# Kernel tuning notes

Hardware: AMD Instinct MI355X
Metric: run time of the kernel (lower is better)

## Reference

```python
import jax, jax.numpy as jnp
import numpy as np

TAU = 0.1
SELF_MASK = 1e6  # added to diagonal of self-distances (y_neg is x)


def _cdist(a, b):
    # pairwise L2 distances, [Na, Nb]; eps keeps sqrt grad finite at 0
    sq = (a * a).sum(-1)[:, None] + (b * b).sum(-1)[None, :] - 2.0 * (a @ b.T)
    return jnp.sqrt(jnp.maximum(sq, 1e-12))


def setup_inputs() -> dict:
    key = jax.random.key(0)
    k1, k2 = jax.random.split(key)
    N, D = 4096, 512
    return {
        "x": jax.random.normal(k1, (N, D), dtype=jnp.float32),
        "y_pos": jax.random.normal(k2, (N, D), dtype=jnp.float32),
    }


def reference(x, y_pos):
    # compute_drift_velocity with y_neg = x (training/loss path)
    N = x.shape[0]
    dist_pos = _cdist(x, y_pos)                      # [N, N]
    dist_neg = _cdist(x, x) + SELF_MASK * jnp.eye(N, dtype=x.dtype)
    logits = -jnp.concatenate([dist_pos, dist_neg], axis=1) / TAU  # [N, 2N]
    # dual normalization: row softmax * column softmax, geometric mean
    A_row = jax.nn.softmax(logits, axis=-1)
    A_col = jax.nn.softmax(logits, axis=0)
    A = jnp.sqrt(A_row * A_col)
    A_pos, A_neg = A[:, :N], A[:, N:]
    drift = A_pos @ y_pos - A_neg @ x                # [N, D]
    return drift
```

## Files before the change

kernel.cpp:

```cpp
#include <hip/hip_runtime.h>
#include <math.h>

#define NN   4096
#define DD   512
#define TWON 8192
#define KSLICE 8

typedef _Float16 half_t;
typedef unsigned short u16;
using half8  = __attribute__((ext_vector_type(8))) half_t;
using short8 = __attribute__((ext_vector_type(8))) short;
using f32x4  = __attribute__((ext_vector_type(4))) float;

__device__ __forceinline__ u16 f2bf(float f) {
    unsigned u = __float_as_uint(f);
    u += 0x7fffu + ((u >> 16) & 1u);
    return (u16)(u >> 16);
}
__device__ __forceinline__ float bf2f(u16 h) {
    return __uint_as_float(((unsigned)h) << 16);
}
__device__ __forceinline__ void gl16(const void* g, void* l) {
    __builtin_amdgcn_global_load_lds(
        (const __attribute__((address_space(1))) void*)g,
        (__attribute__((address_space(3))) void*)l, 16, 0, 0);
}
__device__ __forceinline__ f32x4 mfma16h(half8 a, half8 b, f32x4 c) {
    return __builtin_amdgcn_mfma_f32_16x16x32_f16(a, b, c, 0, 0, 0);
}
__device__ __forceinline__ f32x4 mfma16b(short8 a, short8 b, f32x4 c) {
    return __builtin_amdgcn_mfma_f32_16x16x32_bf16(a, b, c, 0, 0, 0);
}

__global__ __launch_bounds__(64)
void prep_k(const float* __restrict__ x, const float* __restrict__ y,
            half_t* __restrict__ bhi, float* __restrict__ nb) {
    int r = blockIdx.x;
    int l = threadIdx.x;
    const float* src = (r < NN) ? (y + (size_t)r * DD) : (x + (size_t)(r - NN) * DD);
    float4 v0 = *reinterpret_cast<const float4*>(src + l * 8);
    float4 v1 = *reinterpret_cast<const float4*>(src + l * 8 + 4);
    float e[8] = {v0.x, v0.y, v0.z, v0.w, v1.x, v1.y, v1.z, v1.w};
    float s = 0.f;
    half8 h;
    #pragma unroll
    for (int q = 0; q < 8; ++q) {
        s += e[q] * e[q];
        h[q] = (half_t)e[q];
    }
    *reinterpret_cast<half8*>(bhi + (size_t)r * DD + l * 8) = h;
    #pragma unroll
    for (int off = 32; off; off >>= 1) s += __shfl_down(s, off);
    if (l == 0) nb[r] = s;
}

__global__ __launch_bounds__(256)
void b2t_k(const float* __restrict__ x, const float* __restrict__ y, u16* __restrict__ b2t) {
    __shared__ float tl[32][33];
    int k0 = blockIdx.x * 32, d0 = blockIdx.y * 32;
    int tx = threadIdx.x, ty = threadIdx.y;
    const float* src = (k0 < NN) ? y : x;
    int row0 = (k0 < NN) ? k0 : (k0 - NN);
    #pragma unroll
    for (int j = 0; j < 4; ++j)
        tl[ty + 8 * j][tx] = src[(size_t)(row0 + ty + 8 * j) * DD + d0 + tx];
    __syncthreads();
    float sgn = (k0 < NN) ? 1.f : -1.f;
    #pragma unroll
    for (int j = 0; j < 4; ++j) {
        float v = tl[tx][ty + 8 * j] * sgn;
        b2t[(size_t)(d0 + ty + 8 * j) * TWON + k0 + tx] = f2bf(v);
    }
}

__global__ __launch_bounds__(256)
void gemm1_k(const half_t* __restrict__ bhi,
             const float* __restrict__ nb, u16* __restrict__ Ef,
             float* __restrict__ Ct,
             float* __restrict__ rpm, float* __restrict__ rps,
             float* __restrict__ cpm, float* __restrict__ cps) {
    __shared__ unsigned char lds[32768];
    const int t = threadIdx.x;
    const int wave = t >> 6, lane = t & 63;
    const int i0 = blockIdx.y * 128, j0 = blockIdx.x * 128;
    const int wm = (wave >> 1) * 64, wn = (wave & 1) * 64;
    const half_t* ahig = bhi + (size_t)NN * DD;
    f32x4 acc[4][4] = {};
    for (int k0 = 0; k0 < DD; k0 += 64) {
        __syncthreads();
        #pragma unroll
        for (int q = 0; q < 4; ++q) {
            const int dbase = (wave * 4 + q) * 1024;
            const int p  = dbase + lane * 16;
            const int r  = p >> 7;
            const int cb = (p & 127) ^ ((r & 7) << 4);
            const size_t offA = (size_t)(i0 + r) * DD + k0 + (cb >> 1);
            const size_t offB = (size_t)(j0 + r) * DD + k0 + (cb >> 1);
            gl16(ahig + offA, lds + dbase);
            gl16(bhi  + offB, lds + 16384 + dbase);
        }
        asm volatile("s_waitcnt vmcnt(0)" ::: "memory");
        __builtin_amdgcn_sched_barrier(0);
        __syncthreads();
        #pragma unroll
        for (int kk = 0; kk < 2; ++kk) {
            half8 ah[4];
            #pragma unroll
            for (int m = 0; m < 4; ++m) {
                const int row = wm + m * 16 + (lane & 15);
                const int off = row * 128 + ((kk * 64 + (lane >> 4) * 16) ^ ((row & 7) << 4));
                ah[m] = *reinterpret_cast<const half8*>(lds + off);
            }
            #pragma unroll
            for (int n = 0; n < 4; ++n) {
                const int row = wn + n * 16 + (lane & 15);
                const int off = row * 128 + ((kk * 64 + (lane >> 4) * 16) ^ ((row & 7) << 4));
                half8 bh = *reinterpret_cast<const half8*>(lds + 16384 + off);
                #pragma unroll
                for (int m = 0; m < 4; ++m)
                    acc[m][n] = mfma16h(ah[m], bh, acc[m][n]);
            }
        }
    }
    float nbj[4];
    #pragma unroll
    for (int n = 0; n < 4; ++n) nbj[n] = nb[j0 + wn + n * 16 + (lane & 15)];
    float tmax = -3.0e38f;
    #pragma unroll
    for (int m = 0; m < 4; ++m) {
        #pragma unroll
        for (int r4 = 0; r4 < 4; ++r4) {
            const int i = i0 + wm + m * 16 + (lane >> 4) * 4 + r4;
            const float nxi = nb[NN + i];
            #pragma unroll
            for (int n = 0; n < 4; ++n) {
                const int j = j0 + wn + n * 16 + (lane & 15);
                float sq = nxi + nbj[n] - 2.0f * acc[m][n][r4];
                float lg = -10.0f * sqrtf(fmaxf(sq, 1e-12f));
                if (j == i + NN) lg = -1e7f;
                acc[m][n][r4] = lg;
                tmax = fmaxf(tmax, lg);
            }
        }
    }
    #pragma unroll
    for (int off = 1; off < 64; off <<= 1) tmax = fmaxf(tmax, __shfl_xor(tmax, off));
    __syncthreads();
    float* red = reinterpret_cast<float*>(lds);
    if (lane == 0) red[wave] = tmax;
    __syncthreads();
    const float C = fmaxf(fmaxf(red[0], red[1]), fmaxf(red[2], red[3]));
    __syncthreads();
    if (t == 0) Ct[blockIdx.y * 64 + blockIdx.x] = C;
    float rs[16] = {}, cs[4] = {};
    #pragma unroll
    for (int m = 0; m < 4; ++m)
        #pragma unroll
        for (int r4 = 0; r4 < 4; ++r4) {
            const int idx = m * 4 + r4;
            const int i = i0 + wm + m * 16 + (lane >> 4) * 4 + r4;
            #pragma unroll
            for (int n = 0; n < 4; ++n) {
                const int j = j0 + wn + n * 16 + (lane & 15);
                float e = __expf(acc[m][n][r4] - C);
                Ef[(size_t)i * TWON + j] = f2bf(e);
                rs[idx] += e;
                cs[n]   += e;
            }
        }
    #pragma unroll
    for (int off = 1; off < 16; off <<= 1) {
        #pragma unroll
        for (int idx = 0; idx < 16; ++idx) rs[idx] += __shfl_xor(rs[idx], off);
    }
    #pragma unroll
    for (int off = 16; off < 64; off <<= 1) {
        #pragma unroll
        for (int n = 0; n < 4; ++n) cs[n] += __shfl_xor(cs[n], off);
    }
    if ((lane & 15) == 0) {
        #pragma unroll
        for (int m = 0; m < 4; ++m)
            #pragma unroll
            for (int r4 = 0; r4 < 4; ++r4) {
                const int r = wm + m * 16 + (lane >> 4) * 4 + r4;
                red[(wave & 1) * 128 + r] = rs[m * 4 + r4];
            }
    }
    if (lane < 16) {
        #pragma unroll
        for (int n = 0; n < 4; ++n) {
            const int c = wn + n * 16 + lane;
            red[256 + (wave >> 1) * 128 + c] = cs[n];
        }
    }
    __syncthreads();
    if (t < 128) {
        float S = red[t] + red[128 + t];
        rpm[(size_t)blockIdx.x * NN + i0 + t] = C;
        rps[(size_t)blockIdx.x * NN + i0 + t] = S;
    } else {
        const int c = t - 128;
        float S = red[256 + c] + red[384 + c];
        cpm[(size_t)blockIdx.y * TWON + j0 + c] = C;
        cps[(size_t)blockIdx.y * TWON + j0 + c] = S;
    }
}

__global__ __launch_bounds__(256)
void row_comb_k(const float* __restrict__ rpm, const float* __restrict__ rps,
                float* __restrict__ rm, float* __restrict__ rrs) {
    int i = blockIdx.x * 256 + threadIdx.x;
    float M = -3.0e38f;
    for (int tt = 0; tt < TWON / 128; ++tt) M = fmaxf(M, rpm[(size_t)tt * NN + i]);
    float S = 0.f;
    for (int tt = 0; tt < TWON / 128; ++tt)
        S += rps[(size_t)tt * NN + i] * __expf(rpm[(size_t)tt * NN + i] - M);
    rm[i] = M; rrs[i] = rsqrtf(S);
}

__global__ __launch_bounds__(256)
void col_comb_k(const float* __restrict__ cpm, const float* __restrict__ cps,
                float* __restrict__ Pj) {
    int j = blockIdx.x * 256 + threadIdx.x;
    float M = -3.0e38f;
    for (int tt = 0; tt < NN / 128; ++tt) M = fmaxf(M, cpm[(size_t)tt * TWON + j]);
    float S = 0.f;
    for (int tt = 0; tt < NN / 128; ++tt)
        S += cps[(size_t)tt * TWON + j] * __expf(cpm[(size_t)tt * TWON + j] - M);
    Pj[j] = -0.5f * M - 0.5f * logf(S);
}

__global__ __launch_bounds__(512, 4)
void gemm2_k(const u16* __restrict__ Ef, const u16* __restrict__ b2t,
             const float* __restrict__ Ct, const float* __restrict__ rm,
             const float* __restrict__ Pj, const float* __restrict__ rrs,
             float* __restrict__ part) {
    __shared__ unsigned char lds[16384];
    const int t = threadIdx.x;
    const int wave = t >> 6, lane = t & 63;
    const int sw = blockIdx.x;
    const int kslice = sw & 7;
    const int i0 = (sw >> 3) * 64;
    const int ib = (sw >> 3) >> 1;
    const int kbase = kslice * (TWON / KSLICE);
    const int wn = wave * 64;
    const int sr = t >> 3;
    const int kc = (t & 7) * 8;
    const int awbyte = sr * 128 + ((kc * 2) ^ ((sr & 7) << 4));
    const int NT = (TWON / KSLICE) / 64;
    const float rmh = 0.5f * rm[i0 + sr];
    f32x4 acc[4][4] = {};
    short8 aE;
    float4 p0, p1;
    float arg;
    auto LOADA = [&](int it) {
        const int k = kbase + it * 64 + kc;
        aE = *reinterpret_cast<const short8*>(Ef + (size_t)(i0 + sr) * TWON + k);
        p0 = *reinterpret_cast<const float4*>(Pj + k);
        p1 = *reinterpret_cast<const float4*>(Pj + k + 4);
        arg = Ct[ib * 64 + ((kbase + it * 64) >> 7)] - rmh;
    };
    auto STOREA = [&](int buf) {
        short8 g;
        g[0] = (short)f2bf(bf2f((u16)aE[0]) * __expf(arg + p0.x));
        g[1] = (short)f2bf(bf2f((u16)aE[1]) * __expf(arg + p0.y));
        g[2] = (short)f2bf(bf2f((u16)aE[2]) * __expf(arg + p0.z));
        g[3] = (short)f2bf(bf2f((u16)aE[3]) * __expf(arg + p0.w));
        g[4] = (short)f2bf(bf2f((u16)aE[4]) * __expf(arg + p1.x));
        g[5] = (short)f2bf(bf2f((u16)aE[5]) * __expf(arg + p1.y));
        g[6] = (short)f2bf(bf2f((u16)aE[6]) * __expf(arg + p1.z));
        g[7] = (short)f2bf(bf2f((u16)aE[7]) * __expf(arg + p1.w));
        *reinterpret_cast<short8*>(lds + buf * 8192 + awbyte) = g;
    };
    LOADA(0);
    STOREA(0);
    __syncthreads();
    int cur = 0;
    for (int it = 0; it < NT; ++it) {
        short8 bfr0[4], bfr1[4];
        #pragma unroll
        for (int n = 0; n < 4; ++n) {
            const int d = wn + n * 16 + (lane & 15);
            const u16* bp = b2t + (size_t)d * TWON + kbase + it * 64 + (lane >> 4) * 8;
            bfr0[n] = *reinterpret_cast<const short8*>(bp);
            bfr1[n] = *reinterpret_cast<const short8*>(bp + 32);
        }
        if (it + 1 < NT) LOADA(it + 1);
        #pragma unroll
        for (int kk = 0; kk < 2; ++kk) {
            short8 af[4];
            #pragma unroll
            for (int m = 0; m < 4; ++m) {
                const int row = m * 16 + (lane & 15);
                const int off = cur * 8192 + row * 128 +
                                ((kk * 64 + (lane >> 4) * 16) ^ ((row & 7) << 4));
                af[m] = *reinterpret_cast<const short8*>(lds + off);
            }
            #pragma unroll
            for (int m = 0; m < 4; ++m)
                #pragma unroll
                for (int n = 0; n < 4; ++n)
                    acc[m][n] = mfma16b(af[m], (kk == 0) ? bfr0[n] : bfr1[n], acc[m][n]);
        }
        if (it + 1 < NT) STOREA(cur ^ 1);
        __syncthreads();
        cur ^= 1;
    }
    float* pout = part + (size_t)kslice * NN * DD;
    #pragma unroll
    for (int m = 0; m < 4; ++m) {
        float rf[4];
        #pragma unroll
        for (int r4 = 0; r4 < 4; ++r4) rf[r4] = rrs[i0 + m * 16 + (lane >> 4) * 4 + r4];
        #pragma unroll
        for (int n = 0; n < 4; ++n) {
            const int d = wn + n * 16 + (lane & 15);
            #pragma unroll
            for (int r4 = 0; r4 < 4; ++r4) {
                const int i = i0 + m * 16 + (lane >> 4) * 4 + r4;
                pout[(size_t)i * DD + d] = acc[m][n][r4] * rf[r4];
            }
        }
    }
}

__global__ __launch_bounds__(256)
void reduce_k(const float* __restrict__ part, float* __restrict__ out) {
    const size_t e4 = ((size_t)blockIdx.x * 256 + threadIdx.x) * 4;
    float4 a = *reinterpret_cast<const float4*>(part + e4);
    #pragma unroll
    for (int s = 1; s < KSLICE; ++s) {
        float4 b = *reinterpret_cast<const float4*>(part + (size_t)s * NN * DD + e4);
        a.x += b.x; a.y += b.y; a.z += b.z; a.w += b.w;
    }
    *reinterpret_cast<float4*>(out + e4) = a;
}

extern "C" void kernel_launch(void* const* d_in, const int* in_sizes, int n_in,
                              void* d_out, int out_size, void* d_ws, size_t ws_size,
                              hipStream_t stream) {
    const float* x = (const float*)d_in[0];
    const float* y = (const float*)d_in[1];
    float* out = (float*)d_out;

    char* w = (char*)d_ws;
    const size_t OFF_EF   = 0;
    const size_t OFF_BHI  = 67108864;
    const size_t OFF_B2T  = OFF_BHI + 8388608;
    const size_t OFF_PART = OFF_B2T + 8388608;
    const size_t OFF_RPM  = OFF_PART + 67108864;
    const size_t OFF_RPS  = OFF_RPM + 1048576;
    const size_t OFF_CPM  = OFF_RPS + 1048576;
    const size_t OFF_CPS  = OFF_CPM + 1048576;
    const size_t OFF_CT   = OFF_CPS + 1048576;
    const size_t OFF_TAIL = OFF_CT + 65536;

    u16*    Ef   = (u16*)(w + OFF_EF);
    half_t* bhi  = (half_t*)(w + OFF_BHI);
    u16*    b2t  = (u16*)(w + OFF_B2T);
    float*  part = (float*)(w + OFF_PART);
    float*  rpm  = (float*)(w + OFF_RPM);
    float*  rps  = (float*)(w + OFF_RPS);
    float*  cpm  = (float*)(w + OFF_CPM);
    float*  cps  = (float*)(w + OFF_CPS);
    float*  Ct   = (float*)(w + OFF_CT);
    float*  nb   = (float*)(w + OFF_TAIL);
    float*  rm   = nb  + TWON;
    float*  rrs  = rm  + NN;
    float*  Pj   = rrs + NN;

    prep_k<<<TWON, 64, 0, stream>>>(x, y, bhi, nb);
    gemm1_k<<<dim3(TWON / 128, NN / 128), 256, 0, stream>>>(bhi, nb, Ef, Ct,
                                                            rpm, rps, cpm, cps);
    row_comb_k<<<NN / 256, 256, 0, stream>>>(rpm, rps, rm, rrs);
    col_comb_k<<<TWON / 256, 256, 0, stream>>>(cpm, cps, Pj);
    b2t_k<<<dim3(TWON / 32, DD / 32), dim3(32, 8), 0, stream>>>(x, y, b2t);
    gemm2_k<<<512, 512, 0, stream>>>(Ef, b2t, Ct, rm, Pj, rrs, part);
    reduce_k<<<(NN * DD / 4) / 256, 256, 0, stream>>>(part, out);
}
```

Baseline: 188.8 us.

## Store split-K partials in fp16 and unroll gemm2 loop by two

The split-K partial sums written by gemm2 are now stored as fp16 instead of fp32, halving the write and read traffic between gemm2 and the reduction kernel. The reduction kernel now handles 8 elements per thread. The gemm2 main loop is also unrolled by two with separate A-register sets, so the prefetch for a later step overlaps the current MFMA work without a buffer index variable. Storing partials in fp16 reduces accuracy and may overflow if partial values are large.

```diff
diff --git a/kernel.cpp b/kernel.cpp
--- a/kernel.cpp
+++ b/kernel.cpp
@@ -235,7 +235,7 @@
 void gemm2_k(const u16* __restrict__ Ef, const u16* __restrict__ b2t,
              const float* __restrict__ Ct, const float* __restrict__ rm,
              const float* __restrict__ Pj, const float* __restrict__ rrs,
-             float* __restrict__ part) {
+             half_t* __restrict__ part) {
     __shared__ unsigned char lds[16384];
     const int t = threadIdx.x;
     const int wave = t >> 6, lane = t & 63;
@@ -251,49 +251,64 @@
     const int NT = (TWON / KSLICE) / 64;
     const float rmh = 0.5f * rm[i0 + sr];
     f32x4 acc[4][4] = {};
-    short8 aE;
-    float4 p0, p1;
-    float arg;
-    auto LOADA = [&](int it) {
+    short8 aE_A, aE_B;
+    float4 pA0, pA1, pB0, pB1;
+    float argA, argB;
+    auto LOADA_A = [&](int it) {
         const int k = kbase + it * 64 + kc;
-        aE = *reinterpret_cast<const short8*>(Ef + (size_t)(i0 + sr) * TWON + k);
-        p0 = *reinterpret_cast<const float4*>(Pj + k);
-        p1 = *reinterpret_cast<const float4*>(Pj + k + 4);
-        arg = Ct[ib * 64 + ((kbase + it * 64) >> 7)] - rmh;
-    };
-    auto STOREA = [&](int buf) {
+        aE_A = *reinterpret_cast<const short8*>(Ef + (size_t)(i0 + sr) * TWON + k);
+        pA0 = *reinterpret_cast<const float4*>(Pj + k);
+        pA1 = *reinterpret_cast<const float4*>(Pj + k + 4);
+        argA = Ct[ib * 64 + ((kbase + it * 64) >> 7)] - rmh;
+    };
+    auto LOADA_B = [&](int it) {
+        const int k = kbase + it * 64 + kc;
+        aE_B = *reinterpret_cast<const short8*>(Ef + (size_t)(i0 + sr) * TWON + k);
+        pB0 = *reinterpret_cast<const float4*>(Pj + k);
+        pB1 = *reinterpret_cast<const float4*>(Pj + k + 4);
+        argB = Ct[ib * 64 + ((kbase + it * 64) >> 7)] - rmh;
+    };
+    auto STOREA_A = [&](int buf) {
         short8 g;
-        g[0] = (short)f2bf(bf2f((u16)aE[0]) * __expf(arg + p0.x));
-        g[1] = (short)f2bf(bf2f((u16)aE[1]) * __expf(arg + p0.y));
-        g[2] = (short)f2bf(bf2f((u16)aE[2]) * __expf(arg + p0.z));
-        g[3] = (short)f2bf(bf2f((u16)aE[3]) * __expf(arg + p0.w));
-        g[4] = (short)f2bf(bf2f((u16)aE[4]) * __expf(arg + p1.x));
-        g[5] = (short)f2bf(bf2f((u16)aE[5]) * __expf(arg + p1.y));
-        g[6] = (short)f2bf(bf2f((u16)aE[6]) * __expf(arg + p1.z));
-        g[7] = (short)f2bf(bf2f((u16)aE[7]) * __expf(arg + p1.w));
+        g[0] = (short)f2bf(bf2f((u16)aE_A[0]) * __expf(argA + pA0.x));
+        g[1] = (short)f2bf(bf2f((u16)aE_A[1]) * __expf(argA + pA0.y));
+        g[2] = (short)f2bf(bf2f((u16)aE_A[2]) * __expf(argA + pA0.z));
+        g[3] = (short)f2bf(bf2f((u16)aE_A[3]) * __expf(argA + pA0.w));
+        g[4] = (short)f2bf(bf2f((u16)aE_A[4]) * __expf(argA + pA1.x));
+        g[5] = (short)f2bf(bf2f((u16)aE_A[5]) * __expf(argA + pA1.y));
+        g[6] = (short)f2bf(bf2f((u16)aE_A[6]) * __expf(argA + pA1.z));
+        g[7] = (short)f2bf(bf2f((u16)aE_A[7]) * __expf(argA + pA1.w));
         *reinterpret_cast<short8*>(lds + buf * 8192 + awbyte) = g;
     };
-    LOADA(0);
-    STOREA(0);
-    __syncthreads();
-    int cur = 0;
-    for (int it = 0; it < NT; ++it) {
-        short8 bfr0[4], bfr1[4];
+    auto STOREA_B = [&](int buf) {
+        short8 g;
+        g[0] = (short)f2bf(bf2f((u16)aE_B[0]) * __expf(argB + pB0.x));
+        g[1] = (short)f2bf(bf2f((u16)aE_B[1]) * __expf(argB + pB0.y));
+        g[2] = (short)f2bf(bf2f((u16)aE_B[2]) * __expf(argB + pB0.z));
+        g[3] = (short)f2bf(bf2f((u16)aE_B[3]) * __expf(argB + pB0.w));
+        g[4] = (short)f2bf(bf2f((u16)aE_B[4]) * __expf(argB + pB1.x));
+        g[5] = (short)f2bf(bf2f((u16)aE_B[5]) * __expf(argB + pB1.y));
+        g[6] = (short)f2bf(bf2f((u16)aE_B[6]) * __expf(argB + pB1.z));
+        g[7] = (short)f2bf(bf2f((u16)aE_B[7]) * __expf(argB + pB1.w));
+        *reinterpret_cast<short8*>(lds + buf * 8192 + awbyte) = g;
+    };
+    auto BLOAD = [&](int it, short8* b0, short8* b1) {
         #pragma unroll
         for (int n = 0; n < 4; ++n) {
             const int d = wn + n * 16 + (lane & 15);
             const u16* bp = b2t + (size_t)d * TWON + kbase + it * 64 + (lane >> 4) * 8;
-            bfr0[n] = *reinterpret_cast<const short8*>(bp);
-            bfr1[n] = *reinterpret_cast<const short8*>(bp + 32);
-        }
-        if (it + 1 < NT) LOADA(it + 1);
+            b0[n] = *reinterpret_cast<const short8*>(bp);
+            b1[n] = *reinterpret_cast<const short8*>(bp + 32);
+        }
+    };
+    auto DOMFMA = [&](int buf, short8* b0, short8* b1) {
         #pragma unroll
         for (int kk = 0; kk < 2; ++kk) {
             short8 af[4];
             #pragma unroll
             for (int m = 0; m < 4; ++m) {
                 const int row = m * 16 + (lane & 15);
-                const int off = cur * 8192 + row * 128 +
+                const int off = buf * 8192 + row * 128 +
                                 ((kk * 64 + (lane >> 4) * 16) ^ ((row & 7) << 4));
                 af[m] = *reinterpret_cast<const short8*>(lds + off);
             }
@@ -301,13 +316,27 @@
             for (int m = 0; m < 4; ++m)
                 #pragma unroll
                 for (int n = 0; n < 4; ++n)
-                    acc[m][n] = mfma16b(af[m], (kk == 0) ? bfr0[n] : bfr1[n], acc[m][n]);
-        }
-        if (it + 1 < NT) STOREA(cur ^ 1);
+                    acc[m][n] = mfma16b(af[m], (kk == 0) ? b0[n] : b1[n], acc[m][n]);
+        }
+    };
+    LOADA_A(0);
+    LOADA_B(1);
+    STOREA_A(0);
+    __syncthreads();
+    for (int it = 0; it < NT; it += 2) {
+        short8 bfr0[4], bfr1[4];
+        BLOAD(it, bfr0, bfr1);
+        if (it + 2 < NT) LOADA_A(it + 2);
+        DOMFMA(0, bfr0, bfr1);
+        STOREA_B(1);
         __syncthreads();
-        cur ^= 1;
-    }
-    float* pout = part + (size_t)kslice * NN * DD;
+        BLOAD(it + 1, bfr0, bfr1);
+        if (it + 3 < NT) LOADA_B(it + 3);
+        DOMFMA(1, bfr0, bfr1);
+        if (it + 2 < NT) STOREA_A(0);
+        __syncthreads();
+    }
+    half_t* pout = part + (size_t)kslice * NN * DD;
     #pragma unroll
     for (int m = 0; m < 4; ++m) {
         float rf[4];
@@ -319,22 +348,24 @@
             #pragma unroll
             for (int r4 = 0; r4 < 4; ++r4) {
                 const int i = i0 + m * 16 + (lane >> 4) * 4 + r4;
-                pout[(size_t)i * DD + d] = acc[m][n][r4] * rf[r4];
+                pout[(size_t)i * DD + d] = (half_t)(acc[m][n][r4] * rf[r4]);
             }
         }
     }
 }
 
 __global__ __launch_bounds__(256)
-void reduce_k(const float* __restrict__ part, float* __restrict__ out) {
-    const size_t e4 = ((size_t)blockIdx.x * 256 + threadIdx.x) * 4;
-    float4 a = *reinterpret_cast<const float4*>(part + e4);
-    #pragma unroll
-    for (int s = 1; s < KSLICE; ++s) {
-        float4 b = *reinterpret_cast<const float4*>(part + (size_t)s * NN * DD + e4);
-        a.x += b.x; a.y += b.y; a.z += b.z; a.w += b.w;
-    }
-    *reinterpret_cast<float4*>(out + e4) = a;
+void reduce_k(const half_t* __restrict__ part, float* __restrict__ out) {
+    const size_t e8 = ((size_t)blockIdx.x * 256 + threadIdx.x) * 8;
+    float s[8] = {};
+    #pragma unroll
+    for (int sl = 0; sl < KSLICE; ++sl) {
+        half8 v = *reinterpret_cast<const half8*>(part + (size_t)sl * NN * DD + e8);
+        #pragma unroll
+        for (int q = 0; q < 8; ++q) s[q] += (float)v[q];
+    }
+    *reinterpret_cast<float4*>(out + e8)     = make_float4(s[0], s[1], s[2], s[3]);
+    *reinterpret_cast<float4*>(out + e8 + 4) = make_float4(s[4], s[5], s[6], s[7]);
 }
 
 extern "C" void kernel_launch(void* const* d_in, const int* in_sizes, int n_in,
@@ -359,7 +390,7 @@
     u16*    Ef   = (u16*)(w + OFF_EF);
     half_t* bhi  = (half_t*)(w + OFF_BHI);
     u16*    b2t  = (u16*)(w + OFF_B2T);
-    float*  part = (float*)(w + OFF_PART);
+    half_t* part = (half_t*)(w + OFF_PART);
     float*  rpm  = (float*)(w + OFF_RPM);
     float*  rps  = (float*)(w + OFF_RPS);
     float*  cpm  = (float*)(w + OFF_CPM);
@@ -377,5 +408,5 @@
     col_comb_k<<<TWON / 256, 256, 0, stream>>>(cpm, cps, Pj);
     b2t_k<<<dim3(TWON / 32, DD / 32), dim3(32, 8), 0, stream>>>(x, y, b2t);
     gemm2_k<<<512, 512, 0, stream>>>(Ef, b2t, Ct, rm, Pj, rrs, part);
-    reduce_k<<<(NN * DD / 4) / 256, 256, 0, stream>>>(part, out);
-}
+    reduce_k<<<(NN * DD / 8) / 256, 256, 0, stream>>>(part, out);
+}
```

Result: slower. 210.5 us (+11.5%).

## Store split-K partials as packed bf16 in fragment order and read fp16 copy for transpose

Applied to the files above, without the earlier changes.

The split-K partial sums from gemm2 are now written as packed bf16 in a per-thread fragment-contiguous layout with 16-byte stores, which halves partial traffic and replaces strided scalar fp32 stores. The reduce kernel is rewritten to read that layout and scatter fp32 results to the output. The transpose kernel now reads the existing fp16 copy instead of fp32 inputs, halving its read volume. Partials in bf16 lose precision before the final sum, and the transpose now converts fp16 to bf16 rather than fp32 to bf16.

```diff
diff --git a/kernel.cpp b/kernel.cpp
--- a/kernel.cpp
+++ b/kernel.cpp
@@ -55,20 +55,18 @@
 }
 
 __global__ __launch_bounds__(256)
-void b2t_k(const float* __restrict__ x, const float* __restrict__ y, u16* __restrict__ b2t) {
-    __shared__ float tl[32][33];
+void b2tr_k(const half_t* __restrict__ bhi, u16* __restrict__ b2t) {
+    __shared__ half_t tl[32][33];
     int k0 = blockIdx.x * 32, d0 = blockIdx.y * 32;
     int tx = threadIdx.x, ty = threadIdx.y;
-    const float* src = (k0 < NN) ? y : x;
-    int row0 = (k0 < NN) ? k0 : (k0 - NN);
     #pragma unroll
     for (int j = 0; j < 4; ++j)
-        tl[ty + 8 * j][tx] = src[(size_t)(row0 + ty + 8 * j) * DD + d0 + tx];
+        tl[ty + 8 * j][tx] = bhi[(size_t)(k0 + ty + 8 * j) * DD + d0 + tx];
     __syncthreads();
     float sgn = (k0 < NN) ? 1.f : -1.f;
     #pragma unroll
     for (int j = 0; j < 4; ++j) {
-        float v = tl[tx][ty + 8 * j] * sgn;
+        float v = (float)tl[tx][ty + 8 * j] * sgn;
         b2t[(size_t)(d0 + ty + 8 * j) * TWON + k0 + tx] = f2bf(v);
     }
 }
@@ -235,7 +233,7 @@
 void gemm2_k(const u16* __restrict__ Ef, const u16* __restrict__ b2t,
              const float* __restrict__ Ct, const float* __restrict__ rm,
              const float* __restrict__ Pj, const float* __restrict__ rrs,
-             float* __restrict__ part) {
+             unsigned* __restrict__ part) {
     __shared__ unsigned char lds[16384];
     const int t = threadIdx.x;
     const int wave = t >> 6, lane = t & 63;
@@ -307,34 +305,54 @@
         __syncthreads();
         cur ^= 1;
     }
-    float* pout = part + (size_t)kslice * NN * DD;
+    unsigned* pout = part + ((size_t)(kslice * 64 + (sw >> 3)) * 512 + t) * 32;
     #pragma unroll
     for (int m = 0; m < 4; ++m) {
         float rf[4];
         #pragma unroll
         for (int r4 = 0; r4 < 4; ++r4) rf[r4] = rrs[i0 + m * 16 + (lane >> 4) * 4 + r4];
+        unsigned pk[8];
         #pragma unroll
         for (int n = 0; n < 4; ++n) {
-            const int d = wn + n * 16 + (lane & 15);
-            #pragma unroll
-            for (int r4 = 0; r4 < 4; ++r4) {
-                const int i = i0 + m * 16 + (lane >> 4) * 4 + r4;
-                pout[(size_t)i * DD + d] = acc[m][n][r4] * rf[r4];
-            }
-        }
-    }
-}
-
-__global__ __launch_bounds__(256)
-void reduce_k(const float* __restrict__ part, float* __restrict__ out) {
-    const size_t e4 = ((size_t)blockIdx.x * 256 + threadIdx.x) * 4;
-    float4 a = *reinterpret_cast<const float4*>(part + e4);
-    #pragma unroll
-    for (int s = 1; s < KSLICE; ++s) {
-        float4 b = *reinterpret_cast<const float4*>(part + (size_t)s * NN * DD + e4);
-        a.x += b.x; a.y += b.y; a.z += b.z; a.w += b.w;
-    }
-    *reinterpret_cast<float4*>(out + e4) = a;
+            pk[n * 2]     = (unsigned)f2bf(acc[m][n][0] * rf[0]) |
+                            ((unsigned)f2bf(acc[m][n][1] * rf[1]) << 16);
+            pk[n * 2 + 1] = (unsigned)f2bf(acc[m][n][2] * rf[2]) |
+                            ((unsigned)f2bf(acc[m][n][3] * rf[3]) << 16);
+        }
+        *reinterpret_cast<uint4*>(pout + m * 8)     = *reinterpret_cast<uint4*>(pk);
+        *reinterpret_cast<uint4*>(pout + m * 8 + 4) = *reinterpret_cast<uint4*>(pk + 4);
+    }
+}
+
+__global__ __launch_bounds__(512)
+void reduce_k(const unsigned* __restrict__ part, float* __restrict__ out) {
+    const int b = blockIdx.x;
+    const int iblk = b >> 2, mq = b & 3;
+    const int t = threadIdx.x;
+    const int lane = t & 63, wave = t >> 6;
+    float s[16] = {};
+    #pragma unroll
+    for (int ks = 0; ks < KSLICE; ++ks) {
+        const unsigned* p = part + ((size_t)(ks * 64 + iblk) * 512 + t) * 32 + mq * 8;
+        uint4 a = *reinterpret_cast<const uint4*>(p);
+        uint4 c = *reinterpret_cast<const uint4*>(p + 4);
+        unsigned u[8] = {a.x, a.y, a.z, a.w, c.x, c.y, c.z, c.w};
+        #pragma unroll
+        for (int n = 0; n < 4; ++n) {
+            s[n * 4 + 0] += bf2f((u16)(u[n * 2] & 0xffffu));
+            s[n * 4 + 1] += bf2f((u16)(u[n * 2] >> 16));
+            s[n * 4 + 2] += bf2f((u16)(u[n * 2 + 1] & 0xffffu));
+            s[n * 4 + 3] += bf2f((u16)(u[n * 2 + 1] >> 16));
+        }
+    }
+    #pragma unroll
+    for (int n = 0; n < 4; ++n)
+        #pragma unroll
+        for (int r4 = 0; r4 < 4; ++r4) {
+            const int i = iblk * 64 + mq * 16 + (lane >> 4) * 4 + r4;
+            const int d = wave * 64 + n * 16 + (lane & 15);
+            out[(size_t)i * DD + d] = s[n * 4 + r4];
+        }
 }
 
 extern "C" void kernel_launch(void* const* d_in, const int* in_sizes, int n_in,
@@ -356,26 +374,26 @@
     const size_t OFF_CT   = OFF_CPS + 1048576;
     const size_t OFF_TAIL = OFF_CT + 65536;
 
-    u16*    Ef   = (u16*)(w + OFF_EF);
-    half_t* bhi  = (half_t*)(w + OFF_BHI);
-    u16*    b2t  = (u16*)(w + OFF_B2T);
-    float*  part = (float*)(w + OFF_PART);
-    float*  rpm  = (float*)(w + OFF_RPM);
-    float*  rps  = (float*)(w + OFF_RPS);
-    float*  cpm  = (float*)(w + OFF_CPM);
-    float*  cps  = (float*)(w + OFF_CPS);
-    float*  Ct   = (float*)(w + OFF_CT);
-    float*  nb   = (float*)(w + OFF_TAIL);
-    float*  rm   = nb  + TWON;
-    float*  rrs  = rm  + NN;
-    float*  Pj   = rrs + NN;
+    u16*      Ef   = (u16*)(w + OFF_EF);
+    half_t*   bhi  = (half_t*)(w + OFF_BHI);
+    u16*      b2t  = (u16*)(w + OFF_B2T);
+    unsigned* part = (unsigned*)(w + OFF_PART);
+    float*    rpm  = (float*)(w + OFF_RPM);
+    float*    rps  = (float*)(w + OFF_RPS);
+    float*    cpm  = (float*)(w + OFF_CPM);
+    float*    cps  = (float*)(w + OFF_CPS);
+    float*    Ct   = (float*)(w + OFF_CT);
+    float*    nb   = (float*)(w + OFF_TAIL);
+    float*    rm   = nb  + TWON;
+    float*    rrs  = rm  + NN;
+    float*    Pj   = rrs + NN;
 
     prep_k<<<TWON, 64, 0, stream>>>(x, y, bhi, nb);
     gemm1_k<<<dim3(TWON / 128, NN / 128), 256, 0, stream>>>(bhi, nb, Ef, Ct,
                                                             rpm, rps, cpm, cps);
     row_comb_k<<<NN / 256, 256, 0, stream>>>(rpm, rps, rm, rrs);
     col_comb_k<<<TWON / 256, 256, 0, stream>>>(cpm, cps, Pj);
-    b2t_k<<<dim3(TWON / 32, DD / 32), dim3(32, 8), 0, stream>>>(x, y, b2t);
+    b2tr_k<<<dim3(TWON / 32, DD / 32), dim3(32, 8), 0, stream>>>(bhi, b2t);
     gemm2_k<<<512, 512, 0, stream>>>(Ef, b2t, Ct, rm, Pj, rrs, part);
-    reduce_k<<<(NN * DD / 4) / 256, 256, 0, stream>>>(part, out);
-}
+    reduce_k<<<256, 512, 0, stream>>>(part, out);
+}
```

New measurement: 200.5 us. 6.2% more time.
